# Kernel optimization log

Hardware: AMD Instinct MI355X
Metric: run time of the kernel (lower is better)

The kernel has to match this reference:

```python
import jax, jax.numpy as jnp
import numpy as np

B, S, SM, D, H, DFF = 4, 1024, 1024, 1024, 16, 4096
HD = D // H
EPS = 1e-5


def _ln(x, g, b):
    mu = jnp.mean(x, axis=-1, keepdims=True)
    var = jnp.var(x, axis=-1, keepdims=True)
    return (x - mu) * jax.lax.rsqrt(var + EPS) * g + b


def setup_inputs() -> dict:
    key = jax.random.key(0)
    ks = jax.random.split(key, 20)
    w = lambda k, shp: (0.02 * jax.random.normal(k, shp, dtype=jnp.float32))
    return {
        "tgt": jax.random.normal(ks[0], (B, S, D), dtype=jnp.float32),
        "memory": jax.random.normal(ks[1], (B, SM, D), dtype=jnp.float32),
        # self-attn (no bias)
        "Wq": w(ks[2], (D, D)), "Wk": w(ks[3], (D, D)),
        "Wv": w(ks[4], (D, D)), "Wo": w(ks[5], (D, D)),
        # cross-attn nn.MultiheadAttention params
        "mha_in_w": w(ks[6], (3 * D, D)), "mha_in_b": jnp.zeros((3 * D,), jnp.float32),
        "mha_out_w": w(ks[7], (D, D)), "mha_out_b": jnp.zeros((D,), jnp.float32),
        # FFN
        "W1": w(ks[8], (DFF, D)), "b1": jnp.zeros((DFF,), jnp.float32),
        "W2": w(ks[9], (D, DFF)), "b2": jnp.zeros((D,), jnp.float32),
        # LayerNorms
        "g1": jnp.ones((D,), jnp.float32), "be1": jnp.zeros((D,), jnp.float32),
        "g2": jnp.ones((D,), jnp.float32), "be2": jnp.zeros((D,), jnp.float32),
        "g3": jnp.ones((D,), jnp.float32), "be3": jnp.zeros((D,), jnp.float32),
    }


def _self_attn(x, Wq, Wk, Wv, Wo):
    b, s, d = x.shape
    q = (x @ Wq.T).reshape(b, s, H, HD).transpose(0, 2, 1, 3)  # [B,H,S,hd]
    k = (x @ Wk.T).reshape(b, s, H, HD).transpose(0, 2, 1, 3)
    v = (x @ Wv.T).reshape(b, s, H, HD).transpose(0, 2, 1, 3)
    scores = jnp.einsum('bhqd,bhkd->bhqk', q, k) / jnp.sqrt(jnp.float32(HD))
    mask = jnp.triu(jnp.ones((s, s), dtype=bool), k=1)  # diagonal = full_S - S + 1 = 1
    scores = jnp.where(mask, -jnp.inf, scores)
    attn = jax.nn.softmax(scores, axis=-1)
    out = jnp.einsum('bhqk,bhkd->bhqd', attn, v).transpose(0, 2, 1, 3).reshape(b, s, d)
    return out @ Wo.T, k, v


def _cross_attn(q_in, kv_in, in_w, in_b, out_w, out_b):
    Wq, Wk, Wv = jnp.split(in_w, 3, axis=0)
    bq, bk, bv = jnp.split(in_b, 3, axis=0)
    b, s, d = q_in.shape
    sm = kv_in.shape[1]
    q = (q_in @ Wq.T + bq).reshape(b, s, H, HD).transpose(0, 2, 1, 3)
    k = (kv_in @ Wk.T + bk).reshape(b, sm, H, HD).transpose(0, 2, 1, 3)
    v = (kv_in @ Wv.T + bv).reshape(b, sm, H, HD).transpose(0, 2, 1, 3)
    scores = jnp.einsum('bhqd,bhkd->bhqk', q, k) / jnp.sqrt(jnp.float32(HD))
    attn = jax.nn.softmax(scores, axis=-1)
    out = jnp.einsum('bhqk,bhkd->bhqd', attn, v).transpose(0, 2, 1, 3).reshape(b, s, d)
    return out @ out_w.T + out_b


def reference(tgt, memory, Wq, Wk, Wv, Wo, mha_in_w, mha_in_b, mha_out_w, mha_out_b,
              W1, b1, W2, b2, g1, be1, g2, be2, g3, be3):
    # dropout = 0 (eval mode)
    sa_out, sa_k, sa_v = _self_attn(_ln(tgt, g1, be1), Wq, Wk, Wv, Wo)
    x = tgt + sa_out
    ca_out = _cross_attn(_ln(x, g2, be2), memory, mha_in_w, mha_in_b, mha_out_w, mha_out_b)
    x = x + ca_out
    ff = jax.nn.relu(_ln(x, g3, be3) @ W1.T + b1) @ W2.T + b2
    x = x + ff
    return x, sa_k, sa_v
```

## Files before the change

### kernel.cpp

```cpp
#include <hip/hip_runtime.h>

typedef __bf16 bf16_t;
typedef unsigned int u32;
typedef __attribute__((ext_vector_type(8))) __bf16 bf16x8;
typedef __attribute__((ext_vector_type(4))) __bf16 bf16x4;
typedef __attribute__((ext_vector_type(4))) float f32x4;


__device__ __forceinline__ bf16x8 load8f(const float* f) {
    float4 a = *(const float4*)f;
    float4 b = *(const float4*)(f + 4);
    bf16x8 r;
    r[0] = (bf16_t)a.x; r[1] = (bf16_t)a.y; r[2] = (bf16_t)a.z; r[3] = (bf16_t)a.w;
    r[4] = (bf16_t)b.x; r[5] = (bf16_t)b.y; r[6] = (bf16_t)b.z; r[7] = (bf16_t)b.w;
    return r;
}

__device__ __forceinline__ void gll16(const void* g, const void* l) {
    __builtin_amdgcn_global_load_lds(
        (const __attribute__((address_space(1))) u32*)(unsigned long long)g,
        (__attribute__((address_space(3))) u32*)(unsigned int)(unsigned long long)l,
        16, 0, 0);
}

__global__ __launch_bounds__(256) void conv_kernel(
    const float* __restrict__ Wq, const float* __restrict__ Wk,
    const float* __restrict__ Wv, const float* __restrict__ Wo,
    const float* __restrict__ Wio, const float* __restrict__ Woo,
    const float* __restrict__ W1, const float* __restrict__ W2,
    const float* __restrict__ mem, bf16_t* __restrict__ dst)
{
    long e = ((long)blockIdx.x * 256 + threadIdx.x) * 8;
    const float* s; long o;
    if      (e <  1048576) { s = Wq;  o = e; }
    else if (e <  2097152) { s = Wk;  o = e -  1048576; }
    else if (e <  3145728) { s = Wv;  o = e -  2097152; }
    else if (e <  4194304) { s = Wo;  o = e -  3145728; }
    else if (e <  7340032) { s = Wio; o = e -  4194304; }
    else if (e <  8388608) { s = Woo; o = e -  7340032; }
    else if (e < 12582912) { s = W1;  o = e -  8388608; }
    else if (e < 16777216) { s = W2;  o = e - 12582912; }
    else                   { s = mem; o = e - 16777216; }
    *(bf16x8*)&dst[e] = load8f(s + o);
}

__global__ __launch_bounds__(256) void ln_kernel(
    const float* __restrict__ x,
    const float* __restrict__ g, const float* __restrict__ be,
    bf16_t* __restrict__ out)
{
    int row = blockIdx.x, t = threadIdx.x;
    float4 q = *(const float4*)(x + (long)row * 1024 + t * 4);
    float v[4] = {q.x, q.y, q.z, q.w};
    float s = v[0] + v[1] + v[2] + v[3];
    float s2 = v[0]*v[0] + v[1]*v[1] + v[2]*v[2] + v[3]*v[3];
    for (int off = 32; off > 0; off >>= 1) {
        s  += __shfl_down(s, off);
        s2 += __shfl_down(s2, off);
    }
    __shared__ float rs[4], rq[4];
    int w = t >> 6;
    if ((t & 63) == 0) { rs[w] = s; rq[w] = s2; }
    __syncthreads();
    s  = rs[0] + rs[1] + rs[2] + rs[3];
    s2 = rq[0] + rq[1] + rq[2] + rq[3];
    float mean = s * (1.0f / 1024.0f);
    float var  = s2 * (1.0f / 1024.0f) - mean * mean;
    float rstd = rsqrtf(var + 1e-5f);
    int c = t * 4;
    for (int i = 0; i < 4; i++)
        out[(long)row * 1024 + c + i] =
            (bf16_t)((v[i] - mean) * rstd * g[c + i] + be[c + i]);
}

__global__ __launch_bounds__(512, 2) void gemm_big128(
    const bf16_t* __restrict__ A, int lda,
    const bf16_t* __restrict__ Wb, long w_off, int ldw, int K,
    const float* __restrict__ bias, long b_off,
    const float* resid,
    void* o0, void* o1, void* o2, int mode, int N, int do_relu,
    void* o3, void* o4)
{
    __shared__ __align__(16) bf16_t As[3][128 * 64];
    __shared__ __align__(16) bf16_t Bs[3][256 * 64];
    int tid = threadIdx.x;
    int lin = blockIdx.y * gridDim.x + blockIdx.x;
    int mb = lin % gridDim.y, nb = lin / gridDim.y;
    int m0 = mb << 7, n0 = nb << 8;
    int w = tid >> 6, lane = tid & 63;
    int l15 = lane & 15, quad = lane >> 4;
    int wm = w >> 2, wn = w & 3;
    int srow = lane >> 3;
    int cgo  = ((lane & 7) ^ srow) << 3;

    const bf16_t* Wg = Wb + w_off;
    int nk = K >> 6;

    f32x4 acc[4][4];
    #pragma unroll
    for (int i = 0; i < 4; i++)
        #pragma unroll
        for (int j = 0; j < 4; j++)
            acc[i][j] = (f32x4){0.f, 0.f, 0.f, 0.f};

#define STAGEB(P, KK)                                                         \
    _Pragma("unroll")                                                         \
    for (int g = 0; g < 2; g++) {                                             \
        int rg = ((g << 3) + w) << 3;                                         \
        gll16(A  + (long)(m0 + rg + srow) * lda + (KK) + cgo, &As[P][rg << 6]); \
    }                                                                         \
    _Pragma("unroll")                                                         \
    for (int g = 0; g < 4; g++) {                                             \
        int rg = ((g << 3) + w) << 3;                                         \
        gll16(Wg + (long)(n0 + rg + srow) * ldw + (KK) + cgo, &Bs[P][rg << 6]); \
    }

    STAGEB(0, 0)
    if (nk > 1) STAGEB(1, 64)
    if (nk > 1) { asm volatile("s_waitcnt vmcnt(6)"); }
    else        { asm volatile("s_waitcnt vmcnt(0)"); }
    __builtin_amdgcn_sched_barrier(0);
    __builtin_amdgcn_s_barrier();
    __builtin_amdgcn_sched_barrier(0);

    int p = 0;
    for (int t = 0; t < nk; t++) {
        bf16x8 bfr[4][2];
        #pragma unroll
        for (int q = 0; q < 2; q++) {
            bf16x8 af[2][2];
            #pragma unroll
            for (int i2 = 0; i2 < 2; i2++)
                #pragma unroll
                for (int ks = 0; ks < 2; ks++) {
                    int row = (wm << 6) + (((q << 1) + i2) << 4) + l15;
                    int sl = ((quad + (ks << 2)) ^ (l15 & 7)) << 3;
                    af[i2][ks] = *(const bf16x8*)&As[p][(row << 6) + sl];
                }
            if (q == 0) {
                #pragma unroll
                for (int j = 0; j < 4; j++)
                    #pragma unroll
                    for (int ks = 0; ks < 2; ks++) {
                        int row = (wn << 6) + (j << 4) + l15;
                        int sl = ((quad + (ks << 2)) ^ (l15 & 7)) << 3;
                        bfr[j][ks] = *(const bf16x8*)&Bs[p][(row << 6) + sl];
                    }
                if (t + 2 < nk) {
                    int s2 = (p + 2 >= 3) ? p - 1 : p + 2;
                    STAGEB(s2, (t + 2) << 6)
                }
            }
            asm volatile("s_waitcnt lgkmcnt(0)");
            __builtin_amdgcn_sched_barrier(0);
            __builtin_amdgcn_s_setprio(1);
            #pragma unroll
            for (int i2 = 0; i2 < 2; i2++)
                #pragma unroll
                for (int j = 0; j < 4; j++)
                    #pragma unroll
                    for (int ks = 0; ks < 2; ks++)
                        acc[(q << 1) + i2][j] = __builtin_amdgcn_mfma_f32_16x16x32_bf16(
                            af[i2][ks], bfr[j][ks], acc[(q << 1) + i2][j], 0, 0, 0);
            __builtin_amdgcn_s_setprio(0);
            __builtin_amdgcn_sched_barrier(0);
        }
        if (t + 2 < nk)      { asm volatile("s_waitcnt vmcnt(6)"); }
        else if (t + 1 < nk) { asm volatile("s_waitcnt vmcnt(0)"); }
        __builtin_amdgcn_sched_barrier(0);
        __builtin_amdgcn_s_barrier();
        __builtin_amdgcn_sched_barrier(0);
        p = (p == 2) ? 0 : p + 1;
    }
#undef STAGEB

    int rb = quad << 2;
    for (int i = 0; i < 4; i++) {
        for (int j = 0; j < 4; j++) {
            int col = n0 + (wn << 6) + (j << 4) + l15;
            float bv = bias ? bias[b_off + col] : 0.0f;
            int row0 = m0 + (wm << 6) + (i << 4) + rb;
            float vv[4];
            for (int r = 0; r < 4; r++) {
                float v = acc[i][j][r] + bv;
                if (do_relu) v = fmaxf(v, 0.0f);
                vv[r] = v;
            }
            if (mode == 0) {
                for (int r = 0; r < 4; r++) {
                    int row = row0 + r;
                    long idx = (long)row * N + col;
                    float v = vv[r];
                    if (resid) v += resid[idx];
                    if (o0) ((float*)o0)[idx] = v;
                    if (o1) ((bf16_t*)o1)[idx] = (bf16_t)v;
                    if (o2) {
                        long hidx = (((long)(row >> 10) * 16 + (col >> 6)) * 1024
                                     + (row & 1023)) * 64 + (col & 63);
                        ((bf16_t*)o2)[hidx] = (bf16_t)v;
                    }
                }
            } else {
                int seg = col >> 10, c = col & 1023;
                long hb = (long)(row0 >> 10) * 16 + (c >> 6);
                long hidx0 = (hb * 1024 + (row0 & 1023)) * 64 + (c & 63);
                if (mode == 1) {
                    if (seg == 0) {
                        for (int r = 0; r < 4; r++)
                            ((bf16_t*)o0)[hidx0 + r * 64] = (bf16_t)vv[r];
                    } else if (seg == 1) {
                        for (int r = 0; r < 4; r++) {
                            ((float*)o1)[hidx0 + r * 64] = vv[r];
                            if (o3) ((bf16_t*)o3)[hidx0 + r * 64] = (bf16_t)vv[r];
                        }
                    } else {
                        for (int r = 0; r < 4; r++)
                            ((float*)o2)[hidx0 + r * 64] = vv[r];
                        if (o4) {
                            long vt0 = (hb * 64 + (c & 63)) * 1024 + (row0 & 1023);
                            bf16x4 pk;
                            for (int r = 0; r < 4; r++) pk[r] = (bf16_t)vv[r];
                            *(bf16x4*)&((bf16_t*)o4)[vt0] = pk;
                        }
                    }
                } else {
                    if (seg == 0) {
                        for (int r = 0; r < 4; r++)
                            ((bf16_t*)o0)[hidx0 + r * 64] = (bf16_t)vv[r];
                    } else {
                        long vt0 = (hb * 64 + (c & 63)) * 1024 + (row0 & 1023);
                        bf16x4 pk;
                        for (int r = 0; r < 4; r++) pk[r] = (bf16_t)vv[r];
                        *(bf16x4*)&((bf16_t*)o1)[vt0] = pk;
                    }
                }
            }
        }
    }
}

template<int NJ>
__global__ __launch_bounds__(256) void gemm_fast(
    const bf16_t* __restrict__ A, int lda, int a_head,
    const bf16_t* __restrict__ Wb, long w_off, int ldw, int K,
    const float* __restrict__ bias, long b_off,
    const float* resid,
    void* o0, void* o1, void* o2, int mode, int N, int do_relu,
    void* o3, void* o4)
{
    constexpr int BN = NJ << 5;
    __shared__ __align__(16) bf16_t As[3][128 * 64];
    __shared__ __align__(16) bf16_t Bs[3][BN * 64];
    int tid = threadIdx.x;
    int lin = blockIdx.y * gridDim.x + blockIdx.x;
    int mb = lin % gridDim.y, nb = lin / gridDim.y;
    int m0 = mb << 7, n0 = nb * BN;
    int w = tid >> 6, lane = tid & 63;
    int l15 = lane & 15, quad = lane >> 4;
    int wr = (w >> 1) << 6, wc = (w & 1) * (BN >> 1);

    int srow = lane >> 3;
    int cgo  = ((lane & 7) ^ srow) << 3;

    f32x4 acc[4][NJ];
    for (int i = 0; i < 4; i++)
        for (int j = 0; j < NJ; j++)
            acc[i][j] = (f32x4){0.f, 0.f, 0.f, 0.f};

    const bf16_t* Wg = Wb + w_off;
    int nk = K >> 6;

#define STAGE(P, KK)                                                          \
    {                                                                         \
        const bf16_t* Ab; long astr;                                          \
        if (a_head) {                                                         \
            int hh = (KK) >> 6;                                               \
            Ab = A + ((((long)(m0 >> 10)) * 16 + hh) * 1024 + (m0 & 1023)) * 64; \
            astr = 64;                                                        \
        } else {                                                              \
            Ab = A + (long)m0 * lda + (KK);                                   \
            astr = lda;                                                       \
        }                                                                     \
        const bf16_t* Bb = Wg + (long)n0 * ldw + (KK);                        \
        for (int t = 0; t < 4; t++) {                                         \
            int rb2 = (w << 5) + (t << 3);                                    \
            gll16(Ab + (long)(rb2 + srow) * astr + cgo, &As[P][rb2 << 6]);    \
        }                                                                     \
        for (int t = 0; t < NJ; t++) {                                        \
            int rb2 = w * (BN >> 2) + (t << 3);                               \
            gll16(Bb + (long)(rb2 + srow) * ldw + cgo, &Bs[P][rb2 << 6]);     \
        }                                                                     \
    }

#define COMPUTE(P)                                                            \
    for (int ks = 0; ks < 2; ks++) {                                          \
        bf16x8 af[4], bf_[NJ];                                                \
        int gA = quad + (ks << 2);                                            \
        int sl = (gA ^ (l15 & 7)) << 3;                                       \
        for (int i = 0; i < 4; i++)                                           \
            af[i]  = *(const bf16x8*)&As[P][((wr + (i << 4) + l15) << 6) + sl]; \
        for (int j = 0; j < NJ; j++)                                          \
            bf_[j] = *(const bf16x8*)&Bs[P][((wc + (j << 4) + l15) << 6) + sl]; \
        asm volatile("s_waitcnt lgkmcnt(0)");                                 \
        __builtin_amdgcn_sched_barrier(0);                                    \
        __builtin_amdgcn_s_setprio(1);                                        \
        for (int i = 0; i < 4; i++)                                           \
            for (int j = 0; j < NJ; j++)                                      \
                acc[i][j] = __builtin_amdgcn_mfma_f32_16x16x32_bf16(          \
                    af[i], bf_[j], acc[i][j], 0, 0, 0);                       \
        __builtin_amdgcn_s_setprio(0);                                        \
        __builtin_amdgcn_sched_barrier(0);                                    \
    }

    STAGE(0, 0)
    if (nk > 1) STAGE(1, 64)
    if (nk > 1) { asm volatile("s_waitcnt vmcnt(6)"); }
    else        { asm volatile("s_waitcnt vmcnt(0)"); }
    __builtin_amdgcn_sched_barrier(0);
    __builtin_amdgcn_s_barrier();
    __builtin_amdgcn_sched_barrier(0);

    int p = 0;
    for (int kt = 0; kt < nk; kt++) {
        if (kt + 2 < nk) {
            int s2 = (p + 2 >= 3) ? p - 1 : p + 2;
            STAGE(s2, (kt + 2) << 6)
        }
        COMPUTE(p)
        if (kt + 2 < nk)      { asm volatile("s_waitcnt vmcnt(6)"); }
        else if (kt + 1 < nk) { asm volatile("s_waitcnt vmcnt(0)"); }
        __builtin_amdgcn_sched_barrier(0);
        __builtin_amdgcn_s_barrier();
        __builtin_amdgcn_sched_barrier(0);
        p = (p == 2) ? 0 : p + 1;
    }
#undef STAGE
#undef COMPUTE

    int rb = quad << 2;
    for (int i = 0; i < 4; i++) {
        for (int j = 0; j < NJ; j++) {
            int col = n0 + wc + (j << 4) + l15;
            float bv = bias ? bias[b_off + col] : 0.0f;
            for (int r = 0; r < 4; r++) {
                int row = m0 + wr + (i << 4) + rb + r;
                float v = acc[i][j][r] + bv;
                if (do_relu) v = fmaxf(v, 0.0f);
                if (mode == 0) {
                    long idx = (long)row * N + col;
                    if (resid) v += resid[idx];
                    if (o0) ((float*)o0)[idx] = v;
                    if (o1) ((bf16_t*)o1)[idx] = (bf16_t)v;
                    if (o2) {
                        long hidx = (((long)(row >> 10) * 16 + (col >> 6)) * 1024
                                     + (row & 1023)) * 64 + (col & 63);
                        ((bf16_t*)o2)[hidx] = (bf16_t)v;
                    }
                } else {
                    int seg = col >> 10, c = col & 1023;
                    long hidx = (((long)(row >> 10) * 16 + (c >> 6)) * 1024
                                 + (row & 1023)) * 64 + (c & 63);
                    if (mode == 1) {
                        if (seg == 0)      ((bf16_t*)o0)[hidx] = (bf16_t)v;
                        else if (seg == 1) {
                            ((float*)o1)[hidx] = v;
                            if (o3) ((bf16_t*)o3)[hidx] = (bf16_t)v;
                        } else {
                            ((float*)o2)[hidx] = v;
                            if (o4) ((bf16_t*)o4)[hidx] = (bf16_t)v;
                        }
                    } else {
                        if (seg == 0)      ((bf16_t*)o0)[hidx] = (bf16_t)v;
                        else               ((bf16_t*)o1)[hidx] = (bf16_t)v;
                    }
                }
            }
        }
    }
}

#define LDT 40

__global__ __launch_bounds__(256) void gemm_nt(
    const void* __restrict__ A, int lda, int a_head, int a_f32,
    const float* __restrict__ W, long w_off, int ldw,
    int K,
    const float* __restrict__ bias, long b_off,
    const float* __restrict__ resid,
    float*  out_f32, bf16_t* __restrict__ out_b16,
    float*  __restrict__ out_hf32, bf16_t* __restrict__ out_hb16,
    int N, int do_relu)
{
    __shared__ bf16_t As[128 * LDT];
    __shared__ bf16_t Bs[128 * LDT];
    int tid = threadIdx.x;
    int m0 = blockIdx.y << 7, n0 = blockIdx.x << 7;
    int wave = tid >> 6, lane = tid & 63;
    int wr = (wave >> 1) << 6;
    int wc = (wave & 1) << 6;
    int l15 = lane & 15, quad = lane >> 4;

    f32x4 acc[4][4];
    for (int i = 0; i < 4; i++)
        for (int j = 0; j < 4; j++)
            acc[i][j] = (f32x4){0.f, 0.f, 0.f, 0.f};

    int sr = tid >> 2;
    int sc = (tid & 3) << 3;

    for (int k0 = 0; k0 < K; k0 += 32) {
        int kk = k0 + sc;
        long ia0, ia1;
        if (a_head) {
            int hh = kk >> 6, dd = kk & 63;
            int r0g = m0 + sr, r1g = r0g + 64;
            ia0 = ((((long)(r0g >> 10) * 16 + hh) * 1024 + (r0g & 1023)) << 6) + dd;
            ia1 = ((((long)(r1g >> 10) * 16 + hh) * 1024 + (r1g & 1023)) << 6) + dd;
        } else {
            ia0 = (long)(m0 + sr) * lda + kk;
            ia1 = (long)(m0 + sr + 64) * lda + kk;
        }
        long iw0 = w_off + (long)(n0 + sr) * ldw + kk;
        long iw1 = w_off + (long)(n0 + sr + 64) * ldw + kk;
        __syncthreads();
        if (a_f32) {
            *(bf16x8*)&As[sr * LDT + sc]        = load8f((const float*)A + ia0);
            *(bf16x8*)&As[(sr + 64) * LDT + sc] = load8f((const float*)A + ia1);
        } else {
            *(bf16x8*)&As[sr * LDT + sc]        = *(const bf16x8*)((const bf16_t*)A + ia0);
            *(bf16x8*)&As[(sr + 64) * LDT + sc] = *(const bf16x8*)((const bf16_t*)A + ia1);
        }
        *(bf16x8*)&Bs[sr * LDT + sc]        = load8f(W + iw0);
        *(bf16x8*)&Bs[(sr + 64) * LDT + sc] = load8f(W + iw1);
        __syncthreads();
        bf16x8 afr[4], bfr[4];
        for (int i = 0; i < 4; i++)
            afr[i] = *(const bf16x8*)&As[(wr + i * 16 + l15) * LDT + quad * 8];
        for (int j = 0; j < 4; j++)
            bfr[j] = *(const bf16x8*)&Bs[(wc + j * 16 + l15) * LDT + quad * 8];
        for (int i = 0; i < 4; i++)
            for (int j = 0; j < 4; j++)
                acc[i][j] = __builtin_amdgcn_mfma_f32_16x16x32_bf16(
                    afr[i], bfr[j], acc[i][j], 0, 0, 0);
    }

    int rb = quad << 2;
    for (int i = 0; i < 4; i++) {
        for (int j = 0; j < 4; j++) {
            int col = n0 + wc + (j << 4) + l15;
            float bv = bias ? bias[b_off + col] : 0.0f;
            for (int r = 0; r < 4; r++) {
                int row = m0 + wr + (i << 4) + rb + r;
                float v = acc[i][j][r] + bv;
                if (do_relu) v = fmaxf(v, 0.0f);
                long idx = (long)row * N + col;
                if (resid) v += resid[idx];
                if (out_f32) out_f32[idx] = v;
                if (out_b16) out_b16[idx] = (bf16_t)v;
                if (out_hf32 || out_hb16) {
                    int bb = row >> 10, ss = row & 1023, hh = col >> 6, dd = col & 63;
                    long hidx = (((long)bb * 16 + hh) * 1024 + ss) * 64 + dd;
                    if (out_hf32) out_hf32[hidx] = v;
                    if (out_hb16) out_hb16[hidx] = (bf16_t)v;
                }
            }
        }
    }
}

__global__ __launch_bounds__(256) void attn_fast(
    const bf16_t* __restrict__ Q, const bf16_t* __restrict__ K,
    const bf16_t* __restrict__ V, bf16_t* __restrict__ AO,
    int Sk, int causal)
{
    __shared__ __align__(16) bf16_t Ks[64 * 72];
    __shared__ __align__(16) bf16_t Vt[64 * 72];
    __shared__ __align__(16) bf16_t Ps[64 * 72];

    int tid = threadIdx.x;
    int qt = blockIdx.x, bh = blockIdx.y;
    int w = tid >> 6, lane = tid & 63;
    int l15 = lane & 15, quad = lane >> 4;
    int wr = w << 4;
    int rowq = wr + (quad << 2);

    const bf16_t* Qb = Q + ((long)bh * 1024 + (qt << 6)) * 64;
    bf16x8 aq0 = *(const bf16x8*)&Qb[(wr + l15) * 64 + (quad << 3)];
    bf16x8 aq1 = *(const bf16x8*)&Qb[(wr + l15) * 64 + (quad << 3) + 32];

    float m_i[4] = {-1e30f, -1e30f, -1e30f, -1e30f};
    float l_i[4] = {0.f, 0.f, 0.f, 0.f};
    f32x4 o_acc[4];
    for (int j = 0; j < 4; j++) o_acc[j] = (f32x4){0.f, 0.f, 0.f, 0.f};

    int nt = causal ? (qt + 1) : (Sk >> 6);
    long kb = (long)bh * Sk * 64;
    long vb = (long)bh * 64 * Sk;

    int r = tid >> 2, c16 = (tid & 3) << 4;

    bf16x8 kr0, kr1, vr0, vr1;
    {
        const bf16_t* kp = K + kb + (long)r * 64 + c16;
        const bf16_t* vp = V + vb + (long)r * Sk + c16;
        kr0 = *(const bf16x8*)kp;       kr1 = *(const bf16x8*)(kp + 8);
        vr0 = *(const bf16x8*)vp;       vr1 = *(const bf16x8*)(vp + 8);
    }

    for (int kt = 0; kt < nt; kt++) {
        __syncthreads();
        *(bf16x8*)&Ks[r * 72 + c16]     = kr0;
        *(bf16x8*)&Ks[r * 72 + c16 + 8] = kr1;
        *(bf16x8*)&Vt[r * 72 + c16]     = vr0;
        *(bf16x8*)&Vt[r * 72 + c16 + 8] = vr1;
        if (kt + 1 < nt) {
            const bf16_t* kp = K + kb + (((long)(kt + 1) << 6) + r) * 64 + c16;
            const bf16_t* vp = V + vb + (long)r * Sk + ((kt + 1) << 6) + c16;
            kr0 = *(const bf16x8*)kp;   kr1 = *(const bf16x8*)(kp + 8);
            vr0 = *(const bf16x8*)vp;   vr1 = *(const bf16x8*)(vp + 8);
        }
        __syncthreads();

        f32x4 s[4];
        for (int j = 0; j < 4; j++) s[j] = (f32x4){0.f, 0.f, 0.f, 0.f};
        for (int j = 0; j < 4; j++) {
            bf16x8 bk0 = *(const bf16x8*)&Ks[((j << 4) + l15) * 72 + (quad << 3)];
            bf16x8 bk1 = *(const bf16x8*)&Ks[((j << 4) + l15) * 72 + (quad << 3) + 32];
            s[j] = __builtin_amdgcn_mfma_f32_16x16x32_bf16(aq0, bk0, s[j], 0, 0, 0);
            s[j] = __builtin_amdgcn_mfma_f32_16x16x32_bf16(aq1, bk1, s[j], 0, 0, 0);
        }

        int diag = causal && (kt == qt);
        for (int rr = 0; rr < 4; rr++) {
            float sv[4];
            for (int j = 0; j < 4; j++) {
                float x = s[j][rr] * 0.125f;
                if (diag && ((j << 4) + l15 > rowq + rr)) x = -1e30f;
                sv[j] = x;
            }
            float mx = fmaxf(fmaxf(sv[0], sv[1]), fmaxf(sv[2], sv[3]));
            for (int off = 1; off < 16; off <<= 1) mx = fmaxf(mx, __shfl_xor(mx, off));
            float mnew = fmaxf(m_i[rr], mx);
            float alpha = __expf(m_i[rr] - mnew);
            float p0 = __expf(sv[0] - mnew), p1 = __expf(sv[1] - mnew);
            float p2 = __expf(sv[2] - mnew), p3 = __expf(sv[3] - mnew);
            float rsum = p0 + p1 + p2 + p3;
            for (int off = 1; off < 16; off <<= 1) rsum += __shfl_xor(rsum, off);
            m_i[rr] = mnew;
            l_i[rr] = l_i[rr] * alpha + rsum;
            for (int j = 0; j < 4; j++) o_acc[j][rr] *= alpha;
            bf16_t* pr = &Ps[(rowq + rr) * 72 + l15];
            pr[0]  = (bf16_t)p0; pr[16] = (bf16_t)p1;
            pr[32] = (bf16_t)p2; pr[48] = (bf16_t)p3;
        }
        asm volatile("s_waitcnt lgkmcnt(0)" ::: "memory");
        __builtin_amdgcn_sched_barrier(0);

        for (int ks = 0; ks < 2; ks++) {
            int sl = (quad + (ks << 2)) << 3;
            bf16x8 ap = *(const bf16x8*)&Ps[(wr + l15) * 72 + sl];
            for (int j = 0; j < 4; j++) {
                bf16x8 bv = *(const bf16x8*)&Vt[((j << 4) + l15) * 72 + sl];
                o_acc[j] = __builtin_amdgcn_mfma_f32_16x16x32_bf16(ap, bv, o_acc[j], 0, 0, 0);
            }
        }
    }

    bf16_t* Ob = AO + ((long)bh * 1024 + (qt << 6)) * 64;
    for (int rr = 0; rr < 4; rr++) {
        float inv = 1.0f / l_i[rr];
        for (int j = 0; j < 4; j++)
            Ob[(rowq + rr) * 64 + (j << 4) + l15] = (bf16_t)(o_acc[j][rr] * inv);
    }
}

__global__ __launch_bounds__(256) void attn_kernel(
    const bf16_t* __restrict__ Q, const void* __restrict__ K,
    const void* __restrict__ V, bf16_t* __restrict__ AO,
    int Sk, int causal, int kv_f32)
{
    __shared__ __align__(16) bf16_t Qs[64 * 72];
    __shared__ __align__(16) bf16_t Ks[64 * 72];
    __shared__ __align__(16) bf16_t Vt[64 * 72];
    __shared__ __align__(16) bf16_t Ps[64 * 72];

    int tid = threadIdx.x;
    int qt = blockIdx.x, bh = blockIdx.y;
    int w = tid >> 6, lane = tid & 63;
    int l15 = lane & 15, quad = lane >> 4;
    int wr = w << 4;
    int rowq = wr + (quad << 2);

    {
        int r = tid >> 2, c16 = (tid & 3) << 4;
        const bf16_t* Qb = Q + ((long)bh * 1024 + qt * 64) * 64;
        bf16x8 a = *(const bf16x8*)&Qb[r * 64 + c16];
        bf16x8 b = *(const bf16x8*)&Qb[r * 64 + c16 + 8];
        *(bf16x8*)&Qs[r * 72 + c16] = a;
        *(bf16x8*)&Qs[r * 72 + c16 + 8] = b;
    }

    float m_i[4] = {-1e30f, -1e30f, -1e30f, -1e30f};
    float l_i[4] = {0.f, 0.f, 0.f, 0.f};
    f32x4 o_acc[4];
    for (int j = 0; j < 4; j++) o_acc[j] = (f32x4){0.f, 0.f, 0.f, 0.f};

    int nt = causal ? (qt + 1) : (Sk >> 6);
    long kvbase = (long)bh * Sk * 64;

    for (int kt = 0; kt < nt; kt++) {
        __syncthreads();
        {
            int r = tid >> 2, c16 = (tid & 3) << 4;
            long off = kvbase + (long)((kt << 6) + r) * 64 + c16;
            bf16x8 k0, k1, v0, v1;
            if (kv_f32) {
                const float* kp = (const float*)K + off;
                const float* vp = (const float*)V + off;
                k0 = load8f(kp); k1 = load8f(kp + 8);
                v0 = load8f(vp); v1 = load8f(vp + 8);
            } else {
                k0 = *(const bf16x8*)((const bf16_t*)K + off);
                k1 = *(const bf16x8*)((const bf16_t*)K + off + 8);
                v0 = *(const bf16x8*)((const bf16_t*)V + off);
                v1 = *(const bf16x8*)((const bf16_t*)V + off + 8);
            }
            *(bf16x8*)&Ks[r * 72 + c16] = k0;
            *(bf16x8*)&Ks[r * 72 + c16 + 8] = k1;
            for (int i = 0; i < 8; i++) {
                Vt[(c16 + i) * 72 + r]     = v0[i];
                Vt[(c16 + 8 + i) * 72 + r] = v1[i];
            }
        }
        __syncthreads();

        f32x4 s[4];
        for (int j = 0; j < 4; j++) s[j] = (f32x4){0.f, 0.f, 0.f, 0.f};
        for (int ks = 0; ks < 2; ks++) {
            int sl = (quad + (ks << 2)) << 3;
            bf16x8 aq = *(const bf16x8*)&Qs[(wr + l15) * 72 + sl];
            for (int j = 0; j < 4; j++) {
                bf16x8 bk = *(const bf16x8*)&Ks[((j << 4) + l15) * 72 + sl];
                s[j] = __builtin_amdgcn_mfma_f32_16x16x32_bf16(aq, bk, s[j], 0, 0, 0);
            }
        }

        int diag = causal && (kt == qt);
        for (int rr = 0; rr < 4; rr++) {
            float sv[4];
            for (int j = 0; j < 4; j++) {
                float x = s[j][rr] * 0.125f;
                if (diag && ((j << 4) + l15 > rowq + rr)) x = -1e30f;
                sv[j] = x;
            }
            float mx = fmaxf(fmaxf(sv[0], sv[1]), fmaxf(sv[2], sv[3]));
            for (int off = 1; off < 16; off <<= 1) mx = fmaxf(mx, __shfl_xor(mx, off));
            float mnew = fmaxf(m_i[rr], mx);
            float alpha = __expf(m_i[rr] - mnew);
            float p0 = __expf(sv[0] - mnew), p1 = __expf(sv[1] - mnew);
            float p2 = __expf(sv[2] - mnew), p3 = __expf(sv[3] - mnew);
            float rsum = p0 + p1 + p2 + p3;
            for (int off = 1; off < 16; off <<= 1) rsum += __shfl_xor(rsum, off);
            m_i[rr] = mnew;
            l_i[rr] = l_i[rr] * alpha + rsum;
            for (int j = 0; j < 4; j++) o_acc[j][rr] *= alpha;
            bf16_t* pr = &Ps[(rowq + rr) * 72 + l15];
            pr[0]  = (bf16_t)p0; pr[16] = (bf16_t)p1;
            pr[32] = (bf16_t)p2; pr[48] = (bf16_t)p3;
        }
        __syncthreads();

        for (int ks = 0; ks < 2; ks++) {
            int sl = (quad + (ks << 2)) << 3;
            bf16x8 ap = *(const bf16x8*)&Ps[(wr + l15) * 72 + sl];
            for (int j = 0; j < 4; j++) {
                bf16x8 bv = *(const bf16x8*)&Vt[((j << 4) + l15) * 72 + sl];
                o_acc[j] = __builtin_amdgcn_mfma_f32_16x16x32_bf16(ap, bv, o_acc[j], 0, 0, 0);
            }
        }
    }

    bf16_t* Ob = AO + ((long)bh * 1024 + qt * 64) * 64;
    for (int rr = 0; rr < 4; rr++) {
        float inv = 1.0f / l_i[rr];
        for (int j = 0; j < 4; j++)
            Ob[(rowq + rr) * 64 + (j << 4) + l15] = (bf16_t)(o_acc[j][rr] * inv);
    }
}

extern "C" void kernel_launch(void* const* d_in, const int* in_sizes, int n_in,
                              void* d_out, int out_size, void* d_ws, size_t ws_size,
                              hipStream_t stream)
{
    (void)in_sizes; (void)n_in; (void)out_size;
    const float* tgt       = (const float*)d_in[0];
    const float* mem       = (const float*)d_in[1];
    const float* Wq        = (const float*)d_in[2];
    const float* Wk        = (const float*)d_in[3];
    const float* Wv        = (const float*)d_in[4];
    const float* Wo        = (const float*)d_in[5];
    const float* mha_in_w  = (const float*)d_in[6];
    const float* mha_in_b  = (const float*)d_in[7];
    const float* mha_out_w = (const float*)d_in[8];
    const float* mha_out_b = (const float*)d_in[9];
    const float* W1        = (const float*)d_in[10];
    const float* b1        = (const float*)d_in[11];
    const float* W2        = (const float*)d_in[12];
    const float* b2        = (const float*)d_in[13];
    const float* g1        = (const float*)d_in[14];
    const float* be1       = (const float*)d_in[15];
    const float* g2        = (const float*)d_in[16];
    const float* be2       = (const float*)d_in[17];
    const float* g3        = (const float*)d_in[18];
    const float* be3       = (const float*)d_in[19];

    float* out_x = (float*)d_out;
    float* out_k = out_x + (1 << 22);
    float* out_v = out_k + (1 << 22);

    bf16_t* R0 = (bf16_t*)d_ws;
    bf16_t* R1 = R0 + (1 << 22);
    bf16_t* R2 = R1 + (1 << 22);

    dim3 blk(256);
    dim3 blk5(512);
    dim3 gA(16, 64);

    if (ws_size >= ((size_t)96 << 20)) {
        bf16_t* Hff  = R2 + (1 << 22);
        bf16_t* Wb   = (bf16_t*)((char*)d_ws + ((size_t)56 << 20));
        bf16_t* memb = Wb + 16777216;
        bf16_t* saKb = Hff;
        bf16_t* saVb = Hff + (1 << 22);
        const long WO_OFF  = 3145728;
        const long CQ_OFF  = 4194304;
        const long CKV_OFF = 5242880;
        const long CO_OFF  = 7340032;
        const long W1_OFF  = 8388608;
        const long W2_OFF  = 12582912;

        conv_kernel<<<10240, blk, 0, stream>>>(Wq, Wk, Wv, Wo, mha_in_w,
                                               mha_out_w, W1, W2, mem, Wb);

        ln_kernel<<<4096, blk, 0, stream>>>(tgt, g1, be1, R0);
        gemm_big128<<<dim3(12, 32), blk5, 0, stream>>>(R0, 1024, Wb, 0, 1024, 1024,
                                                       nullptr, 0, nullptr,
                                                       R1, out_k, out_v, 1, 3072, 0,
                                                       saKb, saVb);
        attn_fast<<<gA, blk, 0, stream>>>(R1, saKb, saVb, R1, 1024, 1);
        gemm_fast<2><<<dim3(16, 32), blk, 0, stream>>>(R1, 0, 1, Wb, WO_OFF, 1024, 1024,
                                                       nullptr, 0, tgt,
                                                       out_x, nullptr, nullptr, 0, 1024, 0,
                                                       nullptr, nullptr);

        ln_kernel<<<4096, blk, 0, stream>>>(out_x, g2, be2, R0);
        gemm_fast<2><<<dim3(16, 32), blk, 0, stream>>>(R0, 1024, 0, Wb, CQ_OFF, 1024, 1024,
                                                       mha_in_b, 0, nullptr,
                                                       nullptr, nullptr, R1, 0, 1024, 0,
                                                       nullptr, nullptr);
        gemm_big128<<<dim3(8, 32), blk5, 0, stream>>>(memb, 1024, Wb, CKV_OFF, 1024, 1024,
                                                      mha_in_b, 1024, nullptr,
                                                      R2, R0, nullptr, 2, 2048, 0,
                                                      nullptr, nullptr);
        attn_fast<<<gA, blk, 0, stream>>>(R1, R2, R0, R1, 1024, 0);
        gemm_fast<2><<<dim3(16, 32), blk, 0, stream>>>(R1, 0, 1, Wb, CO_OFF, 1024, 1024,
                                                       mha_out_b, 0, out_x,
                                                       out_x, nullptr, nullptr, 0, 1024, 0,
                                                       nullptr, nullptr);

        ln_kernel<<<4096, blk, 0, stream>>>(out_x, g3, be3, R0);
        gemm_big128<<<dim3(16, 32), blk5, 0, stream>>>(R0, 1024, Wb, W1_OFF, 1024, 1024,
                                                       b1, 0, nullptr,
                                                       nullptr, Hff, nullptr, 0, 4096, 1,
                                                       nullptr, nullptr);
        gemm_fast<2><<<dim3(16, 32), blk, 0, stream>>>(Hff, 4096, 0, Wb, W2_OFF, 4096, 4096,
                                                       b2, 0, out_x,
                                                       out_x, nullptr, nullptr, 0, 1024, 0,
                                                       nullptr, nullptr);
        return;
    }

    dim3 gD(8, 32);
    dim3 gF1(32, 16);
    dim3 gF2(8, 16);

    ln_kernel<<<4096, blk, 0, stream>>>(tgt, g1, be1, R0);
    gemm_nt<<<gD, blk, 0, stream>>>(R0, 1024, 0, 0, Wq, 0, 1024, 1024,
                                    nullptr, 0, nullptr, nullptr, nullptr,
                                    nullptr, R1, 1024, 0);
    gemm_nt<<<gD, blk, 0, stream>>>(R0, 1024, 0, 0, Wk, 0, 1024, 1024,
                                    nullptr, 0, nullptr, nullptr, nullptr,
                                    out_k, nullptr, 1024, 0);
    gemm_nt<<<gD, blk, 0, stream>>>(R0, 1024, 0, 0, Wv, 0, 1024, 1024,
                                    nullptr, 0, nullptr, nullptr, nullptr,
                                    out_v, nullptr, 1024, 0);
    attn_kernel<<<gA, blk, 0, stream>>>(R1, out_k, out_v, R1, 1024, 1, 1);
    gemm_nt<<<gD, blk, 0, stream>>>(R1, 0, 1, 0, Wo, 0, 1024, 1024,
                                    nullptr, 0, tgt, out_x, nullptr,
                                    nullptr, nullptr, 1024, 0);

    ln_kernel<<<4096, blk, 0, stream>>>(out_x, g2, be2, R0);
    gemm_nt<<<gD, blk, 0, stream>>>(R0, 1024, 0, 0, mha_in_w, 0, 1024, 1024,
                                    mha_in_b, 0, nullptr, nullptr, nullptr,
                                    nullptr, R1, 1024, 0);
    gemm_nt<<<gD, blk, 0, stream>>>(mem, 1024, 0, 1, mha_in_w, (long)1 << 20, 1024, 1024,
                                    mha_in_b, 1024, nullptr, nullptr, nullptr,
                                    nullptr, R2, 1024, 0);
    gemm_nt<<<gD, blk, 0, stream>>>(mem, 1024, 0, 1, mha_in_w, (long)2 << 20, 1024, 1024,
                                    mha_in_b, 2048, nullptr, nullptr, nullptr,
                                    nullptr, R0, 1024, 0);
    attn_kernel<<<gA, blk, 0, stream>>>(R1, R2, R0, R1, 1024, 0, 0);
    gemm_nt<<<gD, blk, 0, stream>>>(R1, 0, 1, 0, mha_out_w, 0, 1024, 1024,
                                    mha_out_b, 0, out_x, out_x, nullptr,
                                    nullptr, nullptr, 1024, 0);

    ln_kernel<<<4096, blk, 0, stream>>>(out_x, g3, be3, R0);
    for (int c = 0; c < 2; c++) {
        const bf16_t* Ac = R0 + (long)c * 2048 * 1024;
        bf16_t*       Hc = R1;
        float*        Xc = out_x + (long)c * 2048 * 1024;
        gemm_nt<<<gF1, blk, 0, stream>>>(Ac, 1024, 0, 0, W1, 0, 1024, 1024,
                                         b1, 0, nullptr, nullptr, Hc,
                                         nullptr, nullptr, 4096, 1);
        gemm_nt<<<gF2, blk, 0, stream>>>(Hc, 4096, 0, 0, W2, 0, 4096, 4096,
                                         b2, 0, Xc, Xc, nullptr,
                                         nullptr, nullptr, 1024, 0);
    }
}
```

Baseline: 600.9 us.

## Split-K the N=1024 output GEMMs with atomic accumulation into residual

The three N=1024 projection GEMMs (self-attn out, cross-attn out, FFN down) now use a split-K grid along z. Partial sums are atomically added into out_x, which a new seed kernel first fills with tgt so the residual comes for free. This raises block count for these small-N GEMMs to fill more CUs, at the cost of atomic traffic and nondeterministic summation order. The big GEMM's prefetch is also split so A tiles are issued in the first half-iteration and B tiles in the second, spreading load issue across the MFMA phases.

Result: slower. 690.7 us (+14.9%).

```diff
diff --git a/kernel.cpp b/kernel.cpp
--- a/kernel.cpp
+++ b/kernel.cpp
@@ -21,6 +21,13 @@
         (const __attribute__((address_space(1))) u32*)(unsigned long long)g,
         (__attribute__((address_space(3))) u32*)(unsigned int)(unsigned long long)l,
         16, 0, 0);
+}
+
+__global__ __launch_bounds__(256) void seed_kernel(
+    const float* __restrict__ src, float* __restrict__ dst)
+{
+    long i = ((long)blockIdx.x * 256 + threadIdx.x) * 4;
+    *(float4*)&dst[i] = *(const float4*)&src[i];
 }
 
 __global__ __launch_bounds__(256) void conv_kernel(
@@ -103,17 +110,19 @@
         for (int j = 0; j < 4; j++)
             acc[i][j] = (f32x4){0.f, 0.f, 0.f, 0.f};
 
-#define STAGEB(P, KK)                                                         \
+#define STAGEB_A(P, KK)                                                       \
     _Pragma("unroll")                                                         \
     for (int g = 0; g < 2; g++) {                                             \
         int rg = ((g << 3) + w) << 3;                                         \
         gll16(A  + (long)(m0 + rg + srow) * lda + (KK) + cgo, &As[P][rg << 6]); \
-    }                                                                         \
+    }
+#define STAGEB_B(P, KK)                                                       \
     _Pragma("unroll")                                                         \
     for (int g = 0; g < 4; g++) {                                             \
         int rg = ((g << 3) + w) << 3;                                         \
         gll16(Wg + (long)(n0 + rg + srow) * ldw + (KK) + cgo, &Bs[P][rg << 6]); \
     }
+#define STAGEB(P, KK) STAGEB_A(P, KK) STAGEB_B(P, KK)
 
     STAGEB(0, 0)
     if (nk > 1) STAGEB(1, 64)
@@ -126,6 +135,7 @@
     int p = 0;
     for (int t = 0; t < nk; t++) {
         bf16x8 bfr[4][2];
+        int s2 = (p + 2 >= 3) ? p - 1 : p + 2;
         #pragma unroll
         for (int q = 0; q < 2; q++) {
             bf16x8 af[2][2];
@@ -146,10 +156,9 @@
                         int sl = ((quad + (ks << 2)) ^ (l15 & 7)) << 3;
                         bfr[j][ks] = *(const bf16x8*)&Bs[p][(row << 6) + sl];
                     }
-                if (t + 2 < nk) {
-                    int s2 = (p + 2 >= 3) ? p - 1 : p + 2;
-                    STAGEB(s2, (t + 2) << 6)
-                }
+                if (t + 2 < nk) { STAGEB_A(s2, (t + 2) << 6) }
+            } else {
+                if (t + 2 < nk) { STAGEB_B(s2, (t + 2) << 6) }
             }
             asm volatile("s_waitcnt lgkmcnt(0)");
             __builtin_amdgcn_sched_barrier(0);
@@ -173,6 +182,8 @@
         p = (p == 2) ? 0 : p + 1;
     }
 #undef STAGEB
+#undef STAGEB_A
+#undef STAGEB_B
 
     int rb = quad << 2;
     for (int i = 0; i < 4; i++) {
@@ -255,6 +266,7 @@
     int lin = blockIdx.y * gridDim.x + blockIdx.x;
     int mb = lin % gridDim.y, nb = lin / gridDim.y;
     int m0 = mb << 7, n0 = nb * BN;
+    int kb = blockIdx.z * K;
     int w = tid >> 6, lane = tid & 63;
     int l15 = lane & 15, quad = lane >> 4;
     int wr = (w >> 1) << 6, wc = (w & 1) * (BN >> 1);
@@ -272,16 +284,17 @@
 
 #define STAGE(P, KK)                                                          \
     {                                                                         \
+        int kk2 = (KK) + kb;                                                  \
         const bf16_t* Ab; long astr;                                          \
         if (a_head) {                                                         \
-            int hh = (KK) >> 6;                                               \
+            int hh = kk2 >> 6;                                                \
             Ab = A + ((((long)(m0 >> 10)) * 16 + hh) * 1024 + (m0 & 1023)) * 64; \
             astr = 64;                                                        \
         } else {                                                              \
-            Ab = A + (long)m0 * lda + (KK);                                   \
+            Ab = A + (long)m0 * lda + kk2;                                    \
             astr = lda;                                                       \
         }                                                                     \
-        const bf16_t* Bb = Wg + (long)n0 * ldw + (KK);                        \
+        const bf16_t* Bb = Wg + (long)n0 * ldw + kk2;                         \
         for (int t = 0; t < 4; t++) {                                         \
             int rb2 = (w << 5) + (t << 3);                                    \
             gll16(Ab + (long)(rb2 + srow) * astr + cgo, &As[P][rb2 << 6]);    \
@@ -338,15 +351,19 @@
 #undef COMPUTE
 
     int rb = quad << 2;
+    int bz0 = (blockIdx.z == 0);
     for (int i = 0; i < 4; i++) {
         for (int j = 0; j < NJ; j++) {
             int col = n0 + wc + (j << 4) + l15;
-            float bv = bias ? bias[b_off + col] : 0.0f;
+            float bv = (bias && bz0) ? bias[b_off + col] : 0.0f;
             for (int r = 0; r < 4; r++) {
                 int row = m0 + wr + (i << 4) + rb + r;
                 float v = acc[i][j][r] + bv;
                 if (do_relu) v = fmaxf(v, 0.0f);
-                if (mode == 0) {
+                if (mode == 3) {
+                    long idx = (long)row * N + col;
+                    atomicAdd((float*)o0 + idx, v);
+                } else if (mode == 0) {
                     long idx = (long)row * N + col;
                     if (resid) v += resid[idx];
                     if (o0) ((float*)o0)[idx] = v;
@@ -739,6 +756,7 @@
         const long W1_OFF  = 8388608;
         const long W2_OFF  = 12582912;
 
+        seed_kernel<<<4096, blk, 0, stream>>>(tgt, out_x);
         conv_kernel<<<10240, blk, 0, stream>>>(Wq, Wk, Wv, Wo, mha_in_w,
                                                mha_out_w, W1, W2, mem, Wb);
 
@@ -748,10 +766,10 @@
                                                        R1, out_k, out_v, 1, 3072, 0,
                                                        saKb, saVb);
         attn_fast<<<gA, blk, 0, stream>>>(R1, saKb, saVb, R1, 1024, 1);
-        gemm_fast<2><<<dim3(16, 32), blk, 0, stream>>>(R1, 0, 1, Wb, WO_OFF, 1024, 1024,
-                                                       nullptr, 0, tgt,
-                                                       out_x, nullptr, nullptr, 0, 1024, 0,
-                                                       nullptr, nullptr);
+        gemm_fast<2><<<dim3(16, 32, 2), blk, 0, stream>>>(R1, 0, 1, Wb, WO_OFF, 1024, 512,
+                                                          nullptr, 0, nullptr,
+                                                          out_x, nullptr, nullptr, 3, 1024, 0,
+                                                          nullptr, nullptr);
 
         ln_kernel<<<4096, blk, 0, stream>>>(out_x, g2, be2, R0);
         gemm_fast<2><<<dim3(16, 32), blk, 0, stream>>>(R0, 1024, 0, Wb, CQ_OFF, 1024, 1024,
@@ -763,20 +781,20 @@
                                                       R2, R0, nullptr, 2, 2048, 0,
                                                       nullptr, nullptr);
         attn_fast<<<gA, blk, 0, stream>>>(R1, R2, R0, R1, 1024, 0);
-        gemm_fast<2><<<dim3(16, 32), blk, 0, stream>>>(R1, 0, 1, Wb, CO_OFF, 1024, 1024,
-                                                       mha_out_b, 0, out_x,
-                                                       out_x, nullptr, nullptr, 0, 1024, 0,
-                                                       nullptr, nullptr);
+        gemm_fast<2><<<dim3(16, 32, 2), blk, 0, stream>>>(R1, 0, 1, Wb, CO_OFF, 1024, 512,
+                                                          mha_out_b, 0, nullptr,
+                                                          out_x, nullptr, nullptr, 3, 1024, 0,
+                                                          nullptr, nullptr);
 
         ln_kernel<<<4096, blk, 0, stream>>>(out_x, g3, be3, R0);
         gemm_big128<<<dim3(16, 32), blk5, 0, stream>>>(R0, 1024, Wb, W1_OFF, 1024, 1024,
                                                        b1, 0, nullptr,
                                                        nullptr, Hff, nullptr, 0, 4096, 1,
                                                        nullptr, nullptr);
-        gemm_fast<2><<<dim3(16, 32), blk, 0, stream>>>(Hff, 4096, 0, Wb, W2_OFF, 4096, 4096,
-                                                       b2, 0, out_x,
-                                                       out_x, nullptr, nullptr, 0, 1024, 0,
-                                                       nullptr, nullptr);
+        gemm_fast<2><<<dim3(16, 32, 4), blk, 0, stream>>>(Hff, 4096, 0, Wb, W2_OFF, 4096, 1024,
+                                                          b2, 0, nullptr,
+                                                          out_x, nullptr, nullptr, 3, 1024, 0,
+                                                          nullptr, nullptr);
         return;
     }
 
```
